# Kernel tuning notes

Hardware: AMD Instinct MI355X
Metric: run time of the kernel (lower is better)

The kernel has to match this reference:

```python
import jax, jax.numpy as jnp
import numpy as np

N = 100000      # nodes per side (bipartite src/dst sets)
E = 1600000     # edges
D = 64          # input feature dim
C = 64          # output feature dim (heads=1)
DE = 32         # edge feature dim
NEG_SLOPE = 0.2 # PyG GATv2 default negative_slope
EPS = 1e-16     # PyG softmax epsilon


def _gatv2(x_src, x_dst, src, dst, e_attr, Wl, Wr, We, att, bias, n_dst):
    # GATv2Conv (heads=1, add_self_loops=False, eval mode => no dropout)
    xl = x_src @ Wl                                   # [Ns, C]
    xr = x_dst @ Wr                                   # [Nd, C]
    xe = e_attr @ We                                  # [E,  C]
    m = jax.nn.leaky_relu(xl[src] + xr[dst] + xe, NEG_SLOPE)  # [E, C]
    logits = m @ att                                  # [E]
    # segment softmax over incoming edges of each dst node
    mx = jax.ops.segment_max(logits, dst, num_segments=n_dst)
    ex = jnp.exp(logits - mx[dst])
    denom = jax.ops.segment_sum(ex, dst, num_segments=n_dst)
    alpha = ex / (denom[dst] + EPS)                   # [E]
    out = jax.ops.segment_sum(alpha[:, None] * xl[src], dst, num_segments=n_dst)
    return out + bias


def setup_inputs() -> dict:
    key = jax.random.key(0)
    ks = jax.random.split(key, 14)
    s = 0.1
    inp = {
        "x0": jax.random.normal(ks[0], (N, D), jnp.float32),
        "x1": jax.random.normal(ks[1], (N, D), jnp.float32),
        "edge_index": jax.random.randint(ks[2], (2, E), 0, N, dtype=jnp.int32).astype(jnp.int64),
        "edge_attr": jax.random.normal(ks[3], (E, DE), jnp.float32),
        # backward_conv params (output aggregated onto x1 / dst side)
        "Wl_b": jax.random.normal(ks[4], (D, C), jnp.float32) * s,
        "Wr_b": jax.random.normal(ks[5], (D, C), jnp.float32) * s,
        "We_b": jax.random.normal(ks[6], (DE, C), jnp.float32) * s,
        "att_b": jax.random.normal(ks[7], (C,), jnp.float32) * s,
        "b_b": jnp.zeros((C,), jnp.float32),
        # forward_conv params (reversed edges, aggregated onto x0)
        "Wl_f": jax.random.normal(ks[8], (D, C), jnp.float32) * s,
        "Wr_f": jax.random.normal(ks[9], (D, C), jnp.float32) * s,
        "We_f": jax.random.normal(ks[10], (DE, C), jnp.float32) * s,
        "att_f": jax.random.normal(ks[11], (C,), jnp.float32) * s,
        "b_f": jnp.zeros((C,), jnp.float32),
    }
    return inp


def reference(x0, x1, edge_index, edge_attr,
              Wl_b, Wr_b, We_b, att_b, b_b,
              Wl_f, Wr_f, We_f, att_f, b_f):
    src, dst = edge_index[0], edge_index[1]
    # backward_conv(x=(x0, x1), edge_index): aggregate onto x1 nodes
    out_b = _gatv2(x0, x1, src, dst, edge_attr, Wl_b, Wr_b, We_b, att_b, b_b, N)
    # forward_conv(x[::-1]=(x1, x0), edge_index.flip(0)): aggregate onto x0 nodes
    out_f = _gatv2(x1, x0, dst, src, edge_attr, Wl_f, Wr_f, We_f, att_f, b_f, N)
    return (out_b, out_f)
```

## Files before the change

### kernel.cpp

```cpp
#include <hip/hip_runtime.h>


#define NEG_SLOPE 0.2f
#define GAT_EPS 1e-16f

typedef _Float16 f16x8 __attribute__((ext_vector_type(8)));
typedef float f32x4 __attribute__((ext_vector_type(4)));

__device__ __forceinline__ float readlane_f(float v, int lane) {
    return __uint_as_float(__builtin_amdgcn_readlane(__float_as_uint(v), lane));
}

__global__ __launch_bounds__(256) void zero_kernel(int4* __restrict__ p, int n4) {
    int stride = gridDim.x * blockDim.x;
    for (int i = blockIdx.x * blockDim.x + threadIdx.x; i < n4; i += stride)
        p[i] = make_int4(0, 0, 0, 0);
}

__global__ __launch_bounds__(256) void transform_kernel(
    const float* __restrict__ x0, const float* __restrict__ x1,
    const float* __restrict__ Wl_b, const float* __restrict__ Wr_f,
    const float* __restrict__ Wr_b, const float* __restrict__ Wl_f,
    float* __restrict__ xlb, float* __restrict__ xrf,
    float* __restrict__ xrb, float* __restrict__ xlf, int n_nodes)
{
    const int lane   = threadIdx.x & 63;
    const int wave   = blockIdx.x * (blockDim.x >> 6) + (threadIdx.x >> 6);
    const int nwaves = gridDim.x * (blockDim.x >> 6);
    const int half   = nwaves >> 1;
    const int sel    = (wave >= half) ? 1 : 0;
    const int w0     = sel ? (wave - half) : wave;

    const float* __restrict__ x  = sel ? x1   : x0;
    const float* __restrict__ W1 = sel ? Wr_b : Wl_b;
    const float* __restrict__ W2 = sel ? Wl_f : Wr_f;
    float* __restrict__ o1       = sel ? xrb  : xlb;
    float* __restrict__ o2       = sel ? xlf  : xrf;

    float w1[64], w2[64];
#pragma unroll
    for (int k = 0; k < 64; ++k) {
        w1[k] = W1[k * 64 + lane];
        w2[k] = W2[k * 64 + lane];
    }
    for (int n = w0; n < n_nodes; n += half) {
        const float xv = x[(size_t)n * 64 + lane];
        float a1 = 0.f, a2 = 0.f;
#pragma unroll
        for (int k = 0; k < 64; ++k) {
            const float xk = readlane_f(xv, k);
            a1 = fmaf(xk, w1[k], a1);
            a2 = fmaf(xk, w2[k], a2);
        }
        o1[(size_t)n * 64 + lane] = a1;
        o2[(size_t)n * 64 + lane] = a2;
    }
}

__device__ __forceinline__ int ei_stride(const int* __restrict__ ei) {
    int acc = 0;
#pragma unroll
    for (int i = 0; i < 64; ++i) acc |= ei[2 * i + 1];
    return (acc == 0) ? 2 : 1;
}

__global__ __launch_bounds__(256) void hist_kernel(
    const int* __restrict__ ei, int* __restrict__ cnt, int n_nodes, int n_edges)
{
    const int st = ei_stride(ei);
    const int stride = gridDim.x * blockDim.x;
    for (int e = blockIdx.x * blockDim.x + threadIdx.x; e < n_edges; e += stride) {
        int src, dst;
        if (st == 2) {
            src = ((const int2*)ei)[e].x;
            dst = ((const int2*)ei)[n_edges + e].x;
        } else {
            src = ei[e];
            dst = ei[n_edges + e];
        }
        atomicAdd(&cnt[dst], 1);
        atomicAdd(&cnt[n_nodes + src], 1);
    }
}

__global__ __launch_bounds__(256) void scan_partial(
    const int* __restrict__ cnt, int* __restrict__ bsum, int n)
{
    const int base = blockIdx.x * 1024 + threadIdx.x * 4;
    int s = 0;
    if (base + 3 < n) {
        int4 v = *(const int4*)(cnt + base);
        s = v.x + v.y + v.z + v.w;
    } else {
        for (int i = 0; i < 4; ++i) if (base + i < n) s += cnt[base + i];
    }
#pragma unroll
    for (int off = 1; off < 64; off <<= 1) s += __shfl_xor(s, off, 64);
    __shared__ int lds[4];
    if ((threadIdx.x & 63) == 0) lds[threadIdx.x >> 6] = s;
    __syncthreads();
    if (threadIdx.x == 0) bsum[blockIdx.x] = lds[0] + lds[1] + lds[2] + lds[3];
}

__global__ __launch_bounds__(256) void scan_bsums(int* __restrict__ bsum, int nb) {
    __shared__ int lds[256];
    const int t = threadIdx.x;
    const int v = (t < nb) ? bsum[t] : 0;
    lds[t] = v;
    __syncthreads();
    for (int off = 1; off < 256; off <<= 1) {
        int u = (t >= off) ? lds[t - off] : 0;
        __syncthreads();
        lds[t] += u;
        __syncthreads();
    }
    if (t < nb) bsum[t] = lds[t] - v;
}

__global__ __launch_bounds__(256) void scan_expand(
    const int* __restrict__ cnt, const int* __restrict__ bsum,
    int* __restrict__ row, int* __restrict__ cur, int n)
{
    const int base = blockIdx.x * 1024 + threadIdx.x * 4;
    int e0 = 0, e1 = 0, e2 = 0, e3 = 0;
    if (base + 3 < n) {
        int4 v = *(const int4*)(cnt + base);
        e0 = v.x; e1 = v.y; e2 = v.z; e3 = v.w;
    } else {
        if (base + 0 < n) e0 = cnt[base + 0];
        if (base + 1 < n) e1 = cnt[base + 1];
        if (base + 2 < n) e2 = cnt[base + 2];
        if (base + 3 < n) e3 = cnt[base + 3];
    }
    const int s = e0 + e1 + e2 + e3;
    const int lane = threadIdx.x & 63;
    int inc = s;
#pragma unroll
    for (int off = 1; off < 64; off <<= 1) {
        int u = __shfl_up(inc, off, 64);
        if (lane >= off) inc += u;
    }
    __shared__ int wsum[4];
    if (lane == 63) wsum[threadIdx.x >> 6] = inc;
    __syncthreads();
    int woff = 0;
    const int w = threadIdx.x >> 6;
    for (int i = 0; i < w; ++i) woff += wsum[i];

    int r = (inc - s) + woff + bsum[blockIdx.x];
    if (base + 0 < n) { row[base + 0] = r; cur[base + 0] = r; r += e0; }
    if (base + 1 < n) { row[base + 1] = r; cur[base + 1] = r; r += e1; }
    if (base + 2 < n) { row[base + 2] = r; cur[base + 2] = r; r += e2; }
    if (base + 3 < n) { row[base + 3] = r; cur[base + 3] = r; r += e3; }
    if (base < n && base + 4 >= n) row[n] = r;
}

__global__ __launch_bounds__(256) void logit_scatter_kernel(
    const int* __restrict__ ei, const float* __restrict__ ea,
    const float* __restrict__ xlb, const float* __restrict__ xrb,
    const float* __restrict__ xlf, const float* __restrict__ xrf,
    const float* __restrict__ Web, const float* __restrict__ Wef,
    const float* __restrict__ attb, const float* __restrict__ attf,
    int* __restrict__ cur, int2* __restrict__ slots,
    int n_nodes, int n_edges)
{
    const int st   = ei_stride(ei);
    const int lane = threadIdx.x & 63;
    const int wave   = blockIdx.x * (blockDim.x >> 6) + (threadIdx.x >> 6);
    const int nwaves = gridDim.x * (blockDim.x >> 6);
    const int l15 = lane & 15;
    const int lg  = lane >> 4;

    f16x8 wb[4], wf[4];
#pragma unroll
    for (int t = 0; t < 4; ++t) {
#pragma unroll
        for (int j = 0; j < 8; ++j) {
            wb[t][j] = (_Float16)Web[(8 * lg + j) * 64 + 4 * l15 + t];
            wf[t][j] = (_Float16)Wef[(8 * lg + j) * 64 + 4 * l15 + t];
        }
    }
    float atb[4], atf[4];
#pragma unroll
    for (int t = 0; t < 4; ++t) {
        atb[t] = attb[4 * l15 + t];
        atf[t] = attf[4 * l15 + t];
    }

    for (int base = wave * 64; base < n_edges; base += nwaves * 64) {
        const int cnt = min(64, n_edges - base);
        int srcv = 0, dstv = 0;
        if (lane < cnt) {
            if (st == 2) {
                srcv = ((const int2*)ei)[base + lane].x;
                dstv = ((const int2*)ei)[n_edges + base + lane].x;
            } else {
                srcv = ei[base + lane];
                dstv = ei[n_edges + base + lane];
            }
        }
        const int ngr = (cnt + 15) >> 4;

#pragma unroll
        for (int T = 0; T < 4; ++T) {
            if (T >= ngr) break;

            f16x8 af;
            const int arow = base + 16 * T + l15;
            if (arow < n_edges) {
                const float* ap = ea + (size_t)arow * 32 + 8 * lg;
                const f32x4 alo = *(const f32x4*)ap;
                const f32x4 ahi = *(const f32x4*)(ap + 4);
#pragma unroll
                for (int j = 0; j < 4; ++j) {
                    af[j]     = (_Float16)alo[j];
                    af[j + 4] = (_Float16)ahi[j];
                }
            } else {
#pragma unroll
                for (int j = 0; j < 8; ++j) af[j] = (_Float16)0.f;
            }

            int sv[4], dv[4];
#pragma unroll
            for (int r = 0; r < 4; ++r) {
                const int idx = 16 * T + 4 * lg + r;
                sv[r] = __shfl(srcv, idx, 64);
                dv[r] = __shfl(dstv, idx, 64);
            }

            f32x4 glb[4], grb[4], glf[4], grf[4];
#pragma unroll
            for (int r = 0; r < 4; ++r) {
                glb[r] = *(const f32x4*)(xlb + (size_t)sv[r] * 64 + 4 * l15);
                grb[r] = *(const f32x4*)(xrb + (size_t)dv[r] * 64 + 4 * l15);
                glf[r] = *(const f32x4*)(xlf + (size_t)dv[r] * 64 + 4 * l15);
                grf[r] = *(const f32x4*)(xrf + (size_t)sv[r] * 64 + 4 * l15);
            }

            f32x4 cb[4], cf[4];
#pragma unroll
            for (int t = 0; t < 4; ++t) {
                const f32x4 z = {0.f, 0.f, 0.f, 0.f};
                cb[t] = __builtin_amdgcn_mfma_f32_16x16x32_f16(af, wb[t], z, 0, 0, 0);
                cf[t] = __builtin_amdgcn_mfma_f32_16x16x32_f16(af, wf[t], z, 0, 0, 0);
            }

            float Pb[4] = {0.f, 0.f, 0.f, 0.f};
            float Pf[4] = {0.f, 0.f, 0.f, 0.f};
#pragma unroll
            for (int r = 0; r < 4; ++r) {
#pragma unroll
                for (int t = 0; t < 4; ++t) {
                    const float s1 = cb[t][r] + (glb[r][t] + grb[r][t]);
                    const float s2 = cf[t][r] + (glf[r][t] + grf[r][t]);
                    const float u1 = fmaxf(s1, 0.f) + NEG_SLOPE * fminf(s1, 0.f);
                    const float u2 = fmaxf(s2, 0.f) + NEG_SLOPE * fminf(s2, 0.f);
                    Pb[r] = fmaf(u1, atb[t], Pb[r]);
                    Pf[r] = fmaf(u2, atf[t], Pf[r]);
                }
            }
#pragma unroll
            for (int r = 0; r < 4; ++r) {
#pragma unroll
                for (int off = 1; off < 16; off <<= 1) {
                    Pb[r] += __shfl_xor(Pb[r], off, 64);
                    Pf[r] += __shfl_xor(Pf[r], off, 64);
                }
            }

            const int r3 = lane & 3;
            const float Lb = (r3 == 0) ? Pb[0] : (r3 == 1) ? Pb[1] : (r3 == 2) ? Pb[2] : Pb[3];
            const float Lf = (r3 == 0) ? Pf[0] : (r3 == 1) ? Pf[1] : (r3 == 2) ? Pf[2] : Pf[3];
            const int eloc = 16 * T + 4 * lg + r3;
            const int sn = __shfl(srcv, eloc, 64);
            const int dn = __shfl(dstv, eloc, 64);
            if (l15 < 4 && eloc < cnt) {
                const float exb = __expf(Lb);
                const float exf = __expf(Lf);
                const int p = atomicAdd(&cur[dn], 1);
                slots[p] = make_int2(sn, __float_as_int(exb));
                const int q = atomicAdd(&cur[n_nodes + sn], 1);
                slots[q] = make_int2(dn, __float_as_int(exf));
            }
        }
    }
}

__global__ __launch_bounds__(256) void gather_kernel(
    const int* __restrict__ row, const int2* __restrict__ slots,
    const float* __restrict__ xlb, const float* __restrict__ xlf,
    const float* __restrict__ bb, const float* __restrict__ bf,
    float* __restrict__ outb, float* __restrict__ outf, int n_nodes)
{
    const int lane   = threadIdx.x & 63;
    const int wave   = blockIdx.x * (blockDim.x >> 6) + (threadIdx.x >> 6);
    const int nwaves = gridDim.x * (blockDim.x >> 6);
    const float bvb = bb[lane], bvf = bf[lane];
    const int total = 2 * n_nodes;

    for (int seg = wave; seg < total; seg += nwaves) {
        const int dir  = (seg >= n_nodes) ? 1 : 0;
        const int node = dir ? (seg - n_nodes) : seg;
        const float* __restrict__ xls = dir ? xlf : xlb;
        const int start = row[seg], end = row[seg + 1];
        float acc = 0.f, den = 0.f;

        for (int base = start; base < end; base += 64) {
            const int cnt = min(64, end - base);
            const int2 sv = (lane < cnt) ? slots[base + lane] : make_int2(0, 0);
            const int ng = (cnt + 3) >> 2;

            int j0 = 0, j1 = min(1, cnt - 1), j2 = min(2, cnt - 1), j3 = min(3, cnt - 1);
            float ce0 = __uint_as_float(__builtin_amdgcn_readlane(sv.y, j0));
            float ce1 = __uint_as_float(__builtin_amdgcn_readlane(sv.y, j1));
            float ce2 = __uint_as_float(__builtin_amdgcn_readlane(sv.y, j2));
            float ce3 = __uint_as_float(__builtin_amdgcn_readlane(sv.y, j3));
            float cx0 = xls[(size_t)__builtin_amdgcn_readlane(sv.x, j0) * 64 + lane];
            float cx1 = xls[(size_t)__builtin_amdgcn_readlane(sv.x, j1) * 64 + lane];
            float cx2 = xls[(size_t)__builtin_amdgcn_readlane(sv.x, j2) * 64 + lane];
            float cx3 = xls[(size_t)__builtin_amdgcn_readlane(sv.x, j3) * 64 + lane];

            for (int g = 0; g < ng; ++g) {
                float ne0 = ce0, ne1 = ce1, ne2 = ce2, ne3 = ce3;
                float nx0 = cx0, nx1 = cx1, nx2 = cx2, nx3 = cx3;
                if (g + 1 < ng) {
                    const int jb = 4 * (g + 1);
                    const int k0 = jb, k1 = min(jb + 1, cnt - 1),
                              k2 = min(jb + 2, cnt - 1), k3 = min(jb + 3, cnt - 1);
                    ne0 = __uint_as_float(__builtin_amdgcn_readlane(sv.y, k0));
                    ne1 = __uint_as_float(__builtin_amdgcn_readlane(sv.y, k1));
                    ne2 = __uint_as_float(__builtin_amdgcn_readlane(sv.y, k2));
                    ne3 = __uint_as_float(__builtin_amdgcn_readlane(sv.y, k3));
                    nx0 = xls[(size_t)__builtin_amdgcn_readlane(sv.x, k0) * 64 + lane];
                    nx1 = xls[(size_t)__builtin_amdgcn_readlane(sv.x, k1) * 64 + lane];
                    nx2 = xls[(size_t)__builtin_amdgcn_readlane(sv.x, k2) * 64 + lane];
                    nx3 = xls[(size_t)__builtin_amdgcn_readlane(sv.x, k3) * 64 + lane];
                }
                const int jb = 4 * g;
                const float e0 = ce0;
                const float e1 = (jb + 1 < cnt) ? ce1 : 0.f;
                const float e2 = (jb + 2 < cnt) ? ce2 : 0.f;
                const float e3 = (jb + 3 < cnt) ? ce3 : 0.f;
                acc = fmaf(e0, cx0, acc);
                acc = fmaf(e1, cx1, acc);
                acc = fmaf(e2, cx2, acc);
                acc = fmaf(e3, cx3, acc);
                den += (e0 + e1) + (e2 + e3);

                ce0 = ne0; ce1 = ne1; ce2 = ne2; ce3 = ne3;
                cx0 = nx0; cx1 = nx1; cx2 = nx2; cx3 = nx3;
            }
        }
        float* __restrict__ out = dir ? outf : outb;
        out[(size_t)node * 64 + lane] = acc / (den + GAT_EPS) + (dir ? bvf : bvb);
    }
}

extern "C" void kernel_launch(void* const* d_in, const int* in_sizes, int n_in,
                              void* d_out, int out_size, void* d_ws, size_t ws_size,
                              hipStream_t stream) {
    const float* x0   = (const float*)d_in[0];
    const float* x1   = (const float*)d_in[1];
    const int*   ei   = (const int*)  d_in[2];
    const float* ea   = (const float*)d_in[3];
    const float* Wl_b = (const float*)d_in[4];
    const float* Wr_b = (const float*)d_in[5];
    const float* We_b = (const float*)d_in[6];
    const float* at_b = (const float*)d_in[7];
    const float* b_b  = (const float*)d_in[8];
    const float* Wl_f = (const float*)d_in[9];
    const float* Wr_f = (const float*)d_in[10];
    const float* We_f = (const float*)d_in[11];
    const float* at_f = (const float*)d_in[12];
    const float* b_f  = (const float*)d_in[13];

    const int N = in_sizes[0] / 64;
    const int E = in_sizes[3] / 32;
    const size_t N64 = (size_t)N * 64;

    float* ws  = (float*)d_ws;
    float* xlb = ws;
    float* xrb = xlb + N64;
    float* xlf = xrb + N64;
    float* xrf = xlf + N64;
    int* cnt   = (int*)(xrf + N64);
    int* row   = cnt + 2 * N;
    int* cur   = row + (2 * N + 2);
    int* bsum  = cur + 2 * N;
    int2* slots = (int2*)(bsum + 256);

    float* outb = (float*)d_out;
    float* outf = outb + N64;

    const int NB = (2 * N + 1023) >> 10;

    zero_kernel<<<128, 256, 0, stream>>>((int4*)cnt, (2 * N) / 4);

    transform_kernel<<<2048, 256, 0, stream>>>(x0, x1, Wl_b, Wr_f, Wr_b, Wl_f,
                                               xlb, xrf, xrb, xlf, N);

    hist_kernel<<<2048, 256, 0, stream>>>(ei, cnt, N, E);
    scan_partial<<<NB, 256, 0, stream>>>(cnt, bsum, 2 * N);
    scan_bsums<<<1, 256, 0, stream>>>(bsum, NB);
    scan_expand<<<NB, 256, 0, stream>>>(cnt, bsum, row, cur, 2 * N);

    logit_scatter_kernel<<<3125, 256, 0, stream>>>(ei, ea, xlb, xrb, xlf, xrf,
                                                   We_b, We_f, at_b, at_f,
                                                   cur, slots, N, E);

    gather_kernel<<<8192, 256, 0, stream>>>(row, slots, xlb, xlf, b_b, b_f,
                                            outb, outf, N);
}
```

Measured before the change: 961.9 us.

## Store node projections as fp16, interleaved per node for gathered edge loads

The transform kernel now writes the two projections of each node as packed fp16 pairs in one interleaved array per side, plus separate fp16 copies of the source-side features for aggregation. The logit kernel then gathers one 16-byte vector per endpoint instead of four fp32 vectors, and the gather kernel reads half-width features. This roughly halves the random-gather traffic in the edge and aggregation phases. It costs fp16 rounding in the logits and the aggregated outputs, and the edge-group loop is no longer unrolled.

```diff
diff --git a/kernel.cpp b/kernel.cpp
--- a/kernel.cpp
+++ b/kernel.cpp
@@ -9,6 +9,14 @@
 
 __device__ __forceinline__ float readlane_f(float v, int lane) {
     return __uint_as_float(__builtin_amdgcn_readlane(__float_as_uint(v), lane));
+}
+
+__device__ __forceinline__ unsigned pack_f16(float a, float b) {
+    _Float16 ha = (_Float16)a, hb = (_Float16)b;
+    unsigned short ua, ub;
+    __builtin_memcpy(&ua, &ha, 2);
+    __builtin_memcpy(&ub, &hb, 2);
+    return (unsigned)ua | ((unsigned)ub << 16);
 }
 
 __global__ __launch_bounds__(256) void zero_kernel(int4* __restrict__ p, int n4) {
@@ -21,8 +29,8 @@
     const float* __restrict__ x0, const float* __restrict__ x1,
     const float* __restrict__ Wl_b, const float* __restrict__ Wr_f,
     const float* __restrict__ Wr_b, const float* __restrict__ Wl_f,
-    float* __restrict__ xlb, float* __restrict__ xrf,
-    float* __restrict__ xrb, float* __restrict__ xlf, int n_nodes)
+    unsigned* __restrict__ xs, unsigned* __restrict__ xd,
+    _Float16* __restrict__ xlb16, _Float16* __restrict__ xlf16, int n_nodes)
 {
     const int lane   = threadIdx.x & 63;
     const int wave   = blockIdx.x * (blockDim.x >> 6) + (threadIdx.x >> 6);
@@ -34,8 +42,7 @@
     const float* __restrict__ x  = sel ? x1   : x0;
     const float* __restrict__ W1 = sel ? Wr_b : Wl_b;
     const float* __restrict__ W2 = sel ? Wl_f : Wr_f;
-    float* __restrict__ o1       = sel ? xrb  : xlb;
-    float* __restrict__ o2       = sel ? xlf  : xrf;
+    unsigned* __restrict__ xo    = sel ? xd   : xs;
 
     float w1[64], w2[64];
 #pragma unroll
@@ -52,8 +59,9 @@
             a1 = fmaf(xk, w1[k], a1);
             a2 = fmaf(xk, w2[k], a2);
         }
-        o1[(size_t)n * 64 + lane] = a1;
-        o2[(size_t)n * 64 + lane] = a2;
+        xo[(size_t)n * 64 + lane] = pack_f16(a1, a2);
+        if (sel == 0) xlb16[(size_t)n * 64 + lane] = (_Float16)a1;
+        else          xlf16[(size_t)n * 64 + lane] = (_Float16)a2;
     }
 }
 
@@ -157,8 +165,7 @@
 
 __global__ __launch_bounds__(256) void logit_scatter_kernel(
     const int* __restrict__ ei, const float* __restrict__ ea,
-    const float* __restrict__ xlb, const float* __restrict__ xrb,
-    const float* __restrict__ xlf, const float* __restrict__ xrf,
+    const unsigned* __restrict__ xs, const unsigned* __restrict__ xd,
     const float* __restrict__ Web, const float* __restrict__ Wef,
     const float* __restrict__ attb, const float* __restrict__ attf,
     int* __restrict__ cur, int2* __restrict__ slots,
@@ -201,10 +208,7 @@
         }
         const int ngr = (cnt + 15) >> 4;
 
-#pragma unroll
-        for (int T = 0; T < 4; ++T) {
-            if (T >= ngr) break;
-
+        for (int T = 0; T < ngr; ++T) {
             f16x8 af;
             const int arow = base + 16 * T + l15;
             if (arow < n_edges) {
@@ -229,13 +233,11 @@
                 dv[r] = __shfl(dstv, idx, 64);
             }
 
-            f32x4 glb[4], grb[4], glf[4], grf[4];
+            f16x8 su[4], du[4];
 #pragma unroll
             for (int r = 0; r < 4; ++r) {
-                glb[r] = *(const f32x4*)(xlb + (size_t)sv[r] * 64 + 4 * l15);
-                grb[r] = *(const f32x4*)(xrb + (size_t)dv[r] * 64 + 4 * l15);
-                glf[r] = *(const f32x4*)(xlf + (size_t)dv[r] * 64 + 4 * l15);
-                grf[r] = *(const f32x4*)(xrf + (size_t)sv[r] * 64 + 4 * l15);
+                su[r] = *(const f16x8*)(xs + (size_t)sv[r] * 64 + 4 * l15);
+                du[r] = *(const f16x8*)(xd + (size_t)dv[r] * 64 + 4 * l15);
             }
 
             f32x4 cb[4], cf[4];
@@ -252,8 +254,8 @@
             for (int r = 0; r < 4; ++r) {
 #pragma unroll
                 for (int t = 0; t < 4; ++t) {
-                    const float s1 = cb[t][r] + (glb[r][t] + grb[r][t]);
-                    const float s2 = cf[t][r] + (glf[r][t] + grf[r][t]);
+                    const float s1 = cb[t][r] + ((float)su[r][2 * t]     + (float)du[r][2 * t]);
+                    const float s2 = cf[t][r] + ((float)du[r][2 * t + 1] + (float)su[r][2 * t + 1]);
                     const float u1 = fmaxf(s1, 0.f) + NEG_SLOPE * fminf(s1, 0.f);
                     const float u2 = fmaxf(s2, 0.f) + NEG_SLOPE * fminf(s2, 0.f);
                     Pb[r] = fmaf(u1, atb[t], Pb[r]);
@@ -289,7 +291,7 @@
 
 __global__ __launch_bounds__(256) void gather_kernel(
     const int* __restrict__ row, const int2* __restrict__ slots,
-    const float* __restrict__ xlb, const float* __restrict__ xlf,
+    const _Float16* __restrict__ xlb16, const _Float16* __restrict__ xlf16,
     const float* __restrict__ bb, const float* __restrict__ bf,
     float* __restrict__ outb, float* __restrict__ outf, int n_nodes)
 {
@@ -302,7 +304,7 @@
     for (int seg = wave; seg < total; seg += nwaves) {
         const int dir  = (seg >= n_nodes) ? 1 : 0;
         const int node = dir ? (seg - n_nodes) : seg;
-        const float* __restrict__ xls = dir ? xlf : xlb;
+        const _Float16* __restrict__ xls = dir ? xlf16 : xlb16;
         const int start = row[seg], end = row[seg + 1];
         float acc = 0.f, den = 0.f;
 
@@ -316,10 +318,10 @@
             float ce1 = __uint_as_float(__builtin_amdgcn_readlane(sv.y, j1));
             float ce2 = __uint_as_float(__builtin_amdgcn_readlane(sv.y, j2));
             float ce3 = __uint_as_float(__builtin_amdgcn_readlane(sv.y, j3));
-            float cx0 = xls[(size_t)__builtin_amdgcn_readlane(sv.x, j0) * 64 + lane];
-            float cx1 = xls[(size_t)__builtin_amdgcn_readlane(sv.x, j1) * 64 + lane];
-            float cx2 = xls[(size_t)__builtin_amdgcn_readlane(sv.x, j2) * 64 + lane];
-            float cx3 = xls[(size_t)__builtin_amdgcn_readlane(sv.x, j3) * 64 + lane];
+            float cx0 = (float)xls[(size_t)__builtin_amdgcn_readlane(sv.x, j0) * 64 + lane];
+            float cx1 = (float)xls[(size_t)__builtin_amdgcn_readlane(sv.x, j1) * 64 + lane];
+            float cx2 = (float)xls[(size_t)__builtin_amdgcn_readlane(sv.x, j2) * 64 + lane];
+            float cx3 = (float)xls[(size_t)__builtin_amdgcn_readlane(sv.x, j3) * 64 + lane];
 
             for (int g = 0; g < ng; ++g) {
                 float ne0 = ce0, ne1 = ce1, ne2 = ce2, ne3 = ce3;
@@ -332,10 +334,10 @@
                     ne1 = __uint_as_float(__builtin_amdgcn_readlane(sv.y, k1));
                     ne2 = __uint_as_float(__builtin_amdgcn_readlane(sv.y, k2));
                     ne3 = __uint_as_float(__builtin_amdgcn_readlane(sv.y, k3));
-                    nx0 = xls[(size_t)__builtin_amdgcn_readlane(sv.x, k0) * 64 + lane];
-                    nx1 = xls[(size_t)__builtin_amdgcn_readlane(sv.x, k1) * 64 + lane];
-                    nx2 = xls[(size_t)__builtin_amdgcn_readlane(sv.x, k2) * 64 + lane];
-                    nx3 = xls[(size_t)__builtin_amdgcn_readlane(sv.x, k3) * 64 + lane];
+                    nx0 = (float)xls[(size_t)__builtin_amdgcn_readlane(sv.x, k0) * 64 + lane];
+                    nx1 = (float)xls[(size_t)__builtin_amdgcn_readlane(sv.x, k1) * 64 + lane];
+                    nx2 = (float)xls[(size_t)__builtin_amdgcn_readlane(sv.x, k2) * 64 + lane];
+                    nx3 = (float)xls[(size_t)__builtin_amdgcn_readlane(sv.x, k3) * 64 + lane];
                 }
                 const int jb = 4 * g;
                 const float e0 = ce0;
@@ -379,12 +381,12 @@
     const int E = in_sizes[3] / 32;
     const size_t N64 = (size_t)N * 64;
 
-    float* ws  = (float*)d_ws;
-    float* xlb = ws;
-    float* xrb = xlb + N64;
-    float* xlf = xrb + N64;
-    float* xrf = xlf + N64;
-    int* cnt   = (int*)(xrf + N64);
+    unsigned* ws    = (unsigned*)d_ws;
+    unsigned* xs    = ws;
+    unsigned* xd    = xs + N64;
+    _Float16* xlb16 = (_Float16*)(xd + N64);
+    _Float16* xlf16 = xlb16 + N64;
+    int* cnt   = (int*)(xlf16 + N64);
     int* row   = cnt + 2 * N;
     int* cur   = row + (2 * N + 2);
     int* bsum  = cur + 2 * N;
@@ -398,17 +400,17 @@
     zero_kernel<<<128, 256, 0, stream>>>((int4*)cnt, (2 * N) / 4);
 
     transform_kernel<<<2048, 256, 0, stream>>>(x0, x1, Wl_b, Wr_f, Wr_b, Wl_f,
-                                               xlb, xrf, xrb, xlf, N);
+                                               xs, xd, xlb16, xlf16, N);
 
     hist_kernel<<<2048, 256, 0, stream>>>(ei, cnt, N, E);
     scan_partial<<<NB, 256, 0, stream>>>(cnt, bsum, 2 * N);
     scan_bsums<<<1, 256, 0, stream>>>(bsum, NB);
     scan_expand<<<NB, 256, 0, stream>>>(cnt, bsum, row, cur, 2 * N);
 
-    logit_scatter_kernel<<<3125, 256, 0, stream>>>(ei, ea, xlb, xrb, xlf, xrf,
+    logit_scatter_kernel<<<3125, 256, 0, stream>>>(ei, ea, xs, xd,
                                                    We_b, We_f, at_b, at_f,
                                                    cur, slots, N, E);
 
-    gather_kernel<<<8192, 256, 0, stream>>>(row, slots, xlb, xlf, b_b, b_f,
+    gather_kernel<<<8192, 256, 0, stream>>>(row, slots, xlb16, xlf16, b_b, b_f,
                                             outb, outf, N);
 }
```

Result: faster. 864.6 us (-10.1%).
